# Kernel optimization log

Measured on AMD Instinct MI355X. Metric: run time of the kernel, lower is better.

The kernel has to match this reference:

```python
import jax, jax.numpy as jnp
import numpy as np


def _lstm_layer(x, W_ih, W_hh, b_ih, b_hh, reverse=False):
    """Single LSTM layer. x: [T, B, D] -> outputs [T, B, H]. PyTorch gate order i,f,g,o."""
    H = W_hh.shape[-1]
    B = x.shape[1]
    # precompute input contribution for all steps
    xg = jnp.einsum('tbd,gd->tbg', x, W_ih) + b_ih + b_hh  # [T, B, 4H]

    def step(carry, xt):
        h, c = carry
        gates = xt + h @ W_hh.T
        i, f, g, o = jnp.split(gates, 4, axis=-1)
        c = jax.nn.sigmoid(f) * c + jax.nn.sigmoid(i) * jnp.tanh(g)
        h = jax.nn.sigmoid(o) * jnp.tanh(c)
        return (h, c), h

    init = (jnp.zeros((B, H), x.dtype), jnp.zeros((B, H), x.dtype))
    _, hs = jax.lax.scan(step, init, xg, reverse=reverse)
    return hs


def setup_inputs() -> dict:
    key = jax.random.key(0)
    ks = jax.random.split(key, 24)
    B, S, L = 64, 256, 16
    VOCAB, CVOCAB, NCLS = 50000, 128, 50
    E, CE, H = 100, 50, 300
    IN0 = E + CE          # 150, bilstm layer-0 input
    IN1 = 2 * H           # 600, bilstm layer-1 input

    def u(k, shape, fan):
        lim = 1.0 / np.sqrt(fan)
        return jax.random.uniform(k, shape, jnp.float32, -lim, lim)

    inp = {
        'word_ids': jax.random.randint(ks[0], (B, S), 0, VOCAB, jnp.int32),
        'char_ids': jax.random.randint(ks[1], (B, S, L), 0, CVOCAB, jnp.int32),
        'word_embed': jax.random.normal(ks[2], (VOCAB, E), jnp.float32) * 0.1,
        'char_embed': jax.random.normal(ks[3], (CVOCAB, CE), jnp.float32) * 0.1,
        # char LSTM: 2 layers, unidirectional, input==hidden==CE -> stack over layers
        'cWih': u(ks[4], (2, 4 * CE, CE), CE),
        'cWhh': u(ks[5], (2, 4 * CE, CE), CE),
        'cbih': u(ks[6], (2, 4 * CE), CE),
        'cbhh': u(ks[7], (2, 4 * CE), CE),
        # bilstm layer 0: stack over directions [2, ...]
        'b0_Wih': u(ks[8], (2, 4 * H, IN0), H),
        'b0_Whh': u(ks[9], (2, 4 * H, H), H),
        'b0_bih': u(ks[10], (2, 4 * H), H),
        'b0_bhh': u(ks[11], (2, 4 * H), H),
        # bilstm layer 1
        'b1_Wih': u(ks[12], (2, 4 * H, IN1), H),
        'b1_Whh': u(ks[13], (2, 4 * H, H), H),
        'b1_bih': u(ks[14], (2, 4 * H), H),
        'b1_bhh': u(ks[15], (2, 4 * H), H),
        'fcW': u(ks[16], (NCLS, 2 * H), 2 * H),
        'fcb': u(ks[17], (NCLS,), 2 * H),
    }
    return inp


def reference(word_ids, char_ids, word_embed, char_embed, cWih, cWhh, cbih, cbhh,
              b0_Wih, b0_Whh, b0_bih, b0_bhh, b1_Wih, b1_Whh, b1_bih, b1_bhh,
              fcW, fcb):
    B, S, L = char_ids.shape
    CE = char_embed.shape[1]

    # --- char-level path: batch all B*S words through the 2-layer char LSTM ---
    ch = char_embed[char_ids.reshape(B * S, L)]            # [BS, L, CE]
    x = jnp.transpose(ch, (1, 0, 2))                       # [L, BS, CE]
    x = _lstm_layer(x, cWih[0], cWhh[0], cbih[0], cbhh[0])
    x = _lstm_layer(x, cWih[1], cWhh[1], cbih[1], cbhh[1])
    char_feat = x[-1].reshape(B, S, CE)                    # last step of top layer

    # --- word path + concat ---
    emb = word_embed[word_ids]                             # [B, S, E]
    seq = jnp.transpose(jnp.concatenate([emb, char_feat], axis=-1), (1, 0, 2))  # [S, B, 150]

    # --- 2-layer bidirectional LSTM ---
    f0 = _lstm_layer(seq, b0_Wih[0], b0_Whh[0], b0_bih[0], b0_bhh[0])
    r0 = _lstm_layer(seq, b0_Wih[1], b0_Whh[1], b0_bih[1], b0_bhh[1], reverse=True)
    h0 = jnp.concatenate([f0, r0], axis=-1)                # [S, B, 600]
    f1 = _lstm_layer(h0, b1_Wih[0], b1_Whh[0], b1_bih[0], b1_bhh[0])
    r1 = _lstm_layer(h0, b1_Wih[1], b1_Whh[1], b1_bih[1], b1_bhh[1], reverse=True)
    h1 = jnp.concatenate([f1, r1], axis=-1)                # [S, B, 600]

    out = jnp.einsum('sbh,ch->bsc', h1, fcW) + fcb         # [B, S, NCLS]
    return jax.nn.log_softmax(out, axis=-1)
```

## Files before the change

### kernel.cpp

```cpp
#include <hip/hip_runtime.h>

typedef unsigned short u16;
typedef unsigned int   u32;
typedef unsigned long long u64;
typedef __attribute__((ext_vector_type(8))) short bf16x8;
typedef __attribute__((ext_vector_type(4))) float f32x4;

#define MFMA16(a,b,c) __builtin_amdgcn_mfma_f32_16x16x32_bf16((a),(b),(c),0,0,0)

#define NWG   19
#define HP    320
#define GP    304
#define XGB   4096
#define SLOTS 257

static const size_t OFF_XG  = 0;
static const size_t SZ_XG   = (size_t)2*256*NWG*XGB*2;
static const size_t OFF_H0  = OFF_XG + SZ_XG;
static const size_t SZ_HB   = (size_t)2*SLOTS*64*HP*2;
static const size_t OFF_H1  = OFF_H0 + SZ_HB;
static const size_t OFF_CF  = OFF_H1 + SZ_HB;
static const size_t SZ_CF   = (size_t)16384*64*2;
static const size_t OFF_W0  = OFF_CF + SZ_CF;
static const size_t SZ_W0   = (size_t)2432*160*2;
static const size_t OFF_W1  = OFF_W0 + SZ_W0;
static const size_t SZ_W1   = (size_t)2432*640*2;
static const size_t OFF_WFC = OFF_W1 + SZ_W1;
static const size_t SZ_WFC  = (size_t)64*640*2;
static const size_t OFF_B0  = OFF_WFC + SZ_WFC;
static const size_t OFF_B1  = OFF_B0 + 2432*4;
static const size_t OFF_BFC = OFF_B1 + 2432*4;
static const size_t OFF_FL0 = OFF_BFC + 64*4;
static const size_t SZ_FL   = (size_t)2*256*NWG*4;
static const size_t OFF_FL1 = OFF_FL0 + SZ_FL;
static const size_t OFF_DT  = OFF_FL1 + SZ_FL;
static const size_t WS_NEED = OFF_DT + 4;

__device__ __forceinline__ float bf2f(u16 u){ union{u32 i; float f;} v; v.i=(u32)u<<16; return v.f; }
__device__ __forceinline__ u16 f2bf(float f){ union{float f; u32 u;} v; v.f=f; u32 r=v.u+0x7fffu+((v.u>>16)&1u); return (u16)(r>>16); }
__device__ __forceinline__ float sigf(float x){ return __builtin_amdgcn_rcpf(1.f+__builtin_amdgcn_exp2f(-1.4426950408889634f*x)); }
__device__ __forceinline__ float tanhf_(float x){ return 2.f*__builtin_amdgcn_rcpf(1.f+__builtin_amdgcn_exp2f(-2.8853900817779268f*x))-1.f; }
__device__ __forceinline__ float ldf(const void* p, size_t i, bool f32){
  return f32 ? ((const float*)p)[i] : bf2f(((const u16*)p)[i]);
}
__device__ __forceinline__ u16 ldh(const void* p, size_t i, bool f32){
  return f32 ? f2bf(((const float*)p)[i]) : ((const u16*)p)[i];
}

__global__ __launch_bounds__(256,1) void k_detect(const u16* __restrict__ probe, u32* __restrict__ cnt)
{
  int c = 0;
  for (int i = threadIdx.x; i < 65536; i += 256) {
    u16 v = probe[i];
    if (((v >> 7) & 0xFF) == 0xFF) ++c;
  }
  if (c) atomicAdd(cnt, (u32)c);
}

__global__ __launch_bounds__(256,4) void k_prep(
    const void* __restrict__ b0_Wih, const void* __restrict__ b0_bih, const void* __restrict__ b0_bhh,
    const void* __restrict__ b1_Wih, const void* __restrict__ b1_bih, const void* __restrict__ b1_bhh,
    const void* __restrict__ fcW,    const void* __restrict__ fcb,
    u16* __restrict__ W0p, u16* __restrict__ W1p, u16* __restrict__ Wfc,
    float* __restrict__ bias0, float* __restrict__ bias1, float* __restrict__ biasfc,
    const u32* __restrict__ dtf)
{
  const bool isf32 = (*dtf >= 8u);
  const int T0 = 2432*160, T1 = 2432*640, T2 = 64*640;
  const int total = T0 + T1 + T2 + 2432 + 2432 + 64;
  for (int i = blockIdx.x*256 + threadIdx.x; i < total; i += gridDim.x*256) {
    int x = i;
    if (x < T0) {
      int n = x/160, k = x%160;
      int dir = n/1216, cc = n%1216, g = cc/GP, uu = cc%GP;
      W0p[x] = (uu<300 && k<150) ? ldh(b0_Wih, ((size_t)dir*1200 + g*300 + uu)*150 + k, isf32) : (u16)0;
      continue;
    }
    x -= T0;
    if (x < T1) {
      int n = x/640, k = x%640;
      int dir = n/1216, cc = n%1216, g = cc/GP, uu = cc%GP;
      int part = (k>=320), ui = k - part*320;
      W1p[x] = (uu<300 && ui<300) ? ldh(b1_Wih, ((size_t)dir*1200 + g*300 + uu)*600 + part*300 + ui, isf32) : (u16)0;
      continue;
    }
    x -= T1;
    if (x < T2) {
      int n = x/640, k = x%640;
      int part = (k>=320), ui = k - part*320;
      Wfc[x] = (n<50 && ui<300) ? ldh(fcW, (size_t)n*600 + part*300 + ui, isf32) : (u16)0;
      continue;
    }
    x -= T2;
    if (x < 2432) {
      int dir = x/1216, cc = x%1216, g = cc/GP, uu = cc%GP;
      bias0[x] = (uu<300) ? ldf(b0_bih, dir*1200+g*300+uu, isf32) + ldf(b0_bhh, dir*1200+g*300+uu, isf32) : 0.f;
      continue;
    }
    x -= 2432;
    if (x < 2432) {
      int dir = x/1216, cc = x%1216, g = cc/GP, uu = cc%GP;
      bias1[x] = (uu<300) ? ldf(b1_bih, dir*1200+g*300+uu, isf32) + ldf(b1_bhh, dir*1200+g*300+uu, isf32) : 0.f;
      continue;
    }
    x -= 2432;
    biasfc[x] = (x<50) ? ldf(fcb, x, isf32) : 0.f;
  }
}

__global__ __launch_bounds__(256,1) void k_char(
    const int* __restrict__ char_ids, const void* __restrict__ cemb,
    const void* __restrict__ cWih, const void* __restrict__ cWhh,
    const void* __restrict__ cbih, const void* __restrict__ cbhh,
    u16* __restrict__ charfeat, const u32* __restrict__ dtf)
{
  __shared__ u16 emb[128][64];
  __shared__ int ids[16][64];
  __shared__ u16 h0s[64][64];
  __shared__ u16 h1s[64][64];
  const bool isf32 = (*dtf >= 8u);
  const int tid = threadIdx.x;
  const int g0  = blockIdx.x * 64;

  for (int e = tid; e < 128*64; e += 256) {
    int row = e>>6, col = e&63;
    (&emb[0][0])[e] = (col<50) ? ldh(cemb, row*50 + col, isf32) : (u16)0;
  }
  for (int e = tid; e < 1024; e += 256) ids[e&15][e>>4] = char_ids[(size_t)g0*16 + e];
  for (int e = tid; e < 4096; e += 256) { (&h0s[0][0])[e] = 0; (&h1s[0][0])[e] = 0; }
  __syncthreads();

  const int w = tid>>6, lane = tid&63, quad = lane>>4, lcol = lane&15;
  const int u = w*16 + lcol;

  bf16x8 Wf[2][4][4];
  #pragma unroll
  for (int l=0; l<2; ++l)
    #pragma unroll
    for (int g=0; g<4; ++g)
      #pragma unroll
      for (int kt=0; kt<4; ++kt) {
        union { bf16x8 v; u16 h[8]; } t8;
        #pragma unroll
        for (int q=0; q<8; ++q) {
          int k = kt*32 + quad*8 + q;
          u16 val = 0;
          if (u < 50) {
            if (k < 50)                  val = ldh(cWih, l*10000 + (g*50+u)*50 + k, isf32);
            else if (k >= 64 && k < 114) val = ldh(cWhh, l*10000 + (g*50+u)*50 + (k-64), isf32);
          }
          t8.h[q] = val;
        }
        Wf[l][g][kt] = t8.v;
      }
  float bs[2][4];
  #pragma unroll
  for (int l=0; l<2; ++l)
    #pragma unroll
    for (int g=0; g<4; ++g)
      bs[l][g] = (u<50) ? ldf(cbih, l*200+g*50+u, isf32) + ldf(cbhh, l*200+g*50+u, isf32) : 0.f;

  float c0[4][4] = {}; float c1[4][4] = {};
  float h0n[4][4], h1n[4][4];

  for (int t=0; t<16; ++t) {
    #pragma unroll
    for (int m=0; m<4; ++m) {
      f32x4 acc[4];
      #pragma unroll
      for (int g=0; g<4; ++g) acc[g] = (f32x4){bs[0][g], bs[0][g], bs[0][g], bs[0][g]};
      #pragma unroll
      for (int kt=0; kt<4; ++kt) {
        bf16x8 a;
        if (kt < 2) { int id = ids[t][m*16+lcol]; a = *(const bf16x8*)&emb[id][kt*32 + quad*8]; }
        else        { a = *(const bf16x8*)&h0s[m*16+lcol][(kt-2)*32 + quad*8]; }
        #pragma unroll
        for (int g=0; g<4; ++g) acc[g] = MFMA16(a, Wf[0][g][kt], acc[g]);
      }
      #pragma unroll
      for (int r=0; r<4; ++r) {
        float cn = sigf(acc[1][r])*c0[m][r] + sigf(acc[0][r])*tanhf_(acc[2][r]);
        c0[m][r] = cn;
        h0n[m][r] = sigf(acc[3][r]) * tanhf_(cn);
      }
    }
    __syncthreads();
    #pragma unroll
    for (int m=0; m<4; ++m)
      #pragma unroll
      for (int r=0; r<4; ++r) h0s[m*16 + quad*4 + r][u] = f2bf(h0n[m][r]);
    __syncthreads();
    #pragma unroll
    for (int m=0; m<4; ++m) {
      f32x4 acc[4];
      #pragma unroll
      for (int g=0; g<4; ++g) acc[g] = (f32x4){bs[1][g], bs[1][g], bs[1][g], bs[1][g]};
      #pragma unroll
      for (int kt=0; kt<4; ++kt) {
        bf16x8 a = (kt<2) ? *(const bf16x8*)&h0s[m*16+lcol][kt*32 + quad*8]
                          : *(const bf16x8*)&h1s[m*16+lcol][(kt-2)*32 + quad*8];
        #pragma unroll
        for (int g=0; g<4; ++g) acc[g] = MFMA16(a, Wf[1][g][kt], acc[g]);
      }
      #pragma unroll
      for (int r=0; r<4; ++r) {
        float cn = sigf(acc[1][r])*c1[m][r] + sigf(acc[0][r])*tanhf_(acc[2][r]);
        c1[m][r] = cn;
        h1n[m][r] = sigf(acc[3][r]) * tanhf_(cn);
      }
    }
    __syncthreads();
    #pragma unroll
    for (int m=0; m<4; ++m)
      #pragma unroll
      for (int r=0; r<4; ++r) h1s[m*16 + quad*4 + r][u] = f2bf(h1n[m][r]);
    __syncthreads();
  }
  for (int e = tid; e < 4096; e += 256)
    charfeat[(size_t)(g0 + (e>>6))*64 + (e&63)] = (&h1s[0][0])[e];
}

__device__ __forceinline__ size_t xg_addr(int n, int row){
  int dir = n/1216, cc = n%1216, g = cc/GP, cg = cc%GP, jj = cg>>4, uc = cg&15;
  int t = row>>6, b = row&63;
  return (((size_t)dir*256 + t)*NWG + jj)*XGB + (g*16 + uc)*64 + b;
}

__global__ __launch_bounds__(256,2) void k_proj0(
    const int* __restrict__ word_ids, const void* __restrict__ wemb,
    const u16* __restrict__ charfeat, const u16* __restrict__ W0p,
    const float* __restrict__ bias0, u16* __restrict__ xg, const u32* __restrict__ dtf)
{
  __shared__ u16 As[64][160];
  __shared__ u16 Bst[64][160];
  const bool isf32 = (*dtf >= 8u);
  const int tid = threadIdx.x;
  const int r0 = blockIdx.x*64, n0 = blockIdx.y*64;
  u32* Asu = (u32*)&As[0][0];
  u32* Bsu = (u32*)&Bst[0][0];
  for (int e = tid; e < 64*80; e += 256) {
    int rr = e/80, cu = e%80;
    int r = r0 + rr, t = r>>6, b = r&63;
    u32 v;
    if (cu < 50) {
      int wid = word_ids[b*256 + t];
      if (isf32) {
        const float* wf = (const float*)wemb;
        v = (u32)f2bf(wf[(size_t)wid*100 + cu*2]) | ((u32)f2bf(wf[(size_t)wid*100 + cu*2 + 1]) << 16);
      } else {
        v = ((const u32*)wemb)[(size_t)wid*50 + cu];
      }
    }
    else if (cu < 75) { v = ((const u32*)charfeat)[(size_t)r*32 + (cu-50)]; }
    else              v = 0;
    Asu[rr*80 + cu] = v;
  }
  for (int e = tid; e < 64*80; e += 256) {
    int n = e/80, cu = e%80;
    Bsu[n*80 + cu] = ((const u32*)W0p)[(size_t)(n0+n)*80 + cu];
  }
  __syncthreads();
  const int w = tid>>6, lane = tid&63, quad = lane>>4, lcol = lane&15;
  f32x4 acc[4] = {};
  #pragma unroll
  for (int kt=0; kt<5; ++kt) {
    bf16x8 a = *(const bf16x8*)&As[w*16+lcol][kt*32 + quad*8];
    #pragma unroll
    for (int nt=0; nt<4; ++nt) {
      bf16x8 bb = *(const bf16x8*)&Bst[nt*16+lcol][kt*32 + quad*8];
      acc[nt] = MFMA16(a, bb, acc[nt]);
    }
  }
  #pragma unroll
  for (int nt=0; nt<4; ++nt) {
    int n = n0 + nt*16 + lcol;
    float bia = bias0[n];
    #pragma unroll
    for (int r=0; r<4; ++r) {
      int row = r0 + w*16 + quad*4 + r;
      xg[xg_addr(n, row)] = f2bf(acc[nt][r] + bia);
    }
  }
}

__global__ __launch_bounds__(256,2) void k_proj1(
    const u16* __restrict__ Hbuf, const u16* __restrict__ W1p,
    const float* __restrict__ bias1, u16* __restrict__ xg)
{
  __shared__ u16 As[64][128];
  __shared__ u16 Bst[64][128];
  const int tid = threadIdx.x;
  const int r0 = blockIdx.x*64, n0 = blockIdx.y*64;
  const u32* Hu = (const u32*)Hbuf;
  const u32* Wu = (const u32*)W1p;
  u32* Asu = (u32*)&As[0][0];
  u32* Bsu = (u32*)&Bst[0][0];
  const int w = tid>>6, lane = tid&63, quad = lane>>4, lcol = lane&15;
  f32x4 acc[4] = {};
  for (int ch=0; ch<5; ++ch) {
    __syncthreads();
    for (int e = tid; e < 4096; e += 256) {
      int rr = e>>6, cu = e&63;
      int r = r0 + rr, t = r>>6, b = r&63;
      int kk = ch*128 + cu*2;
      int part = (kk>=320), off = kk - part*320;
      Asu[e] = Hu[(((size_t)part*SLOTS + (part ? 256-t : t+1))*64 + b)*160 + (off>>1)];
    }
    for (int e = tid; e < 4096; e += 256) {
      int n = e>>6, cu = e&63;
      Bsu[e] = Wu[(size_t)(n0+n)*320 + ch*64 + cu];
    }
    __syncthreads();
    #pragma unroll
    for (int kt=0; kt<4; ++kt) {
      bf16x8 a = *(const bf16x8*)&As[w*16+lcol][kt*32 + quad*8];
      #pragma unroll
      for (int nt=0; nt<4; ++nt) {
        bf16x8 bb = *(const bf16x8*)&Bst[nt*16+lcol][kt*32 + quad*8];
        acc[nt] = MFMA16(a, bb, acc[nt]);
      }
    }
  }
  #pragma unroll
  for (int nt=0; nt<4; ++nt) {
    int n = n0 + nt*16 + lcol;
    float bia = bias1[n];
    #pragma unroll
    for (int r=0; r<4; ++r) {
      int row = r0 + w*16 + quad*4 + r;
      xg[xg_addr(n, row)] = f2bf(acc[nt][r] + bia);
    }
  }
}

__global__ __launch_bounds__(256,1) void k_scan(
    const u16* __restrict__ xg, const void* __restrict__ Whh,
    u16* __restrict__ Hbuf, u32* __restrict__ flags, const u32* __restrict__ dtf)
{
  const bool isf32 = (*dtf >= 8u);
  const int bx = blockIdx.x;
  const int d = bx / NWG, j = bx % NWG;
  const int tid = threadIdx.x;
  const int w = tid>>6, lane = tid&63, quad = lane>>4, lcol = lane&15;
  const int u = j*16 + lcol;
  const int brow = w*16;

  bf16x8 Bf[4][10];
  #pragma unroll
  for (int g=0; g<4; ++g)
    #pragma unroll
    for (int kt=0; kt<10; ++kt) {
      union { bf16x8 v; u16 h[8]; } t8;
      #pragma unroll
      for (int q=0; q<8; ++q) {
        int k = kt*32 + quad*8 + q;
        t8.h[q] = (u < 300 && k < 300) ? ldh(Whh, ((size_t)d*1200 + g*300 + u)*300 + k, isf32) : (u16)0;
      }
      Bf[g][kt] = t8.v;
    }

  float c[4] = {0.f,0.f,0.f,0.f};
  u32* flg = flags + (size_t)d*256*NWG;

  for (int t=0; t<256; ++t) {
    const int tt = d ? (255 - t) : t;
    const volatile u64* xp = (const volatile u64*)(xg + (((size_t)d*256 + tt)*NWG + j)*XGB);
    u64 xq[4];
    #pragma unroll
    for (int g=0; g<4; ++g)
      xq[g] = xp[((g*16 + lcol)*64 + brow + quad*4) >> 2];

    if (t > 0) {
      const u32* f = flg + (t-1)*NWG;
      while (true) {
        u32 v = 4u;
        if (lane < NWG)
          v = __hip_atomic_load(f + lane, __ATOMIC_RELAXED, __HIP_MEMORY_SCOPE_AGENT);
        if (__ballot(v >= 4u) == ~0ull) break;
        __builtin_amdgcn_s_sleep(2);
      }
      asm volatile("" ::: "memory");
    }

    f32x4 acc[4];
    #pragma unroll
    for (int g=0; g<4; ++g) {
      union { u64 q; u16 h[4]; } t4; t4.q = xq[g];
      #pragma unroll
      for (int r=0; r<4; ++r) acc[g][r] = bf2f(t4.h[r]);
    }
    #pragma unroll
    for (int kt=0; kt<10; ++kt) {
      size_t base = (((size_t)d*SLOTS + t)*64 + (brow + lcol))*HP + kt*32 + quad*8;
      union { bf16x8 v; u64 q[2]; } a;
      a.q[0] = __hip_atomic_load((u64*)(Hbuf + base),     __ATOMIC_RELAXED, __HIP_MEMORY_SCOPE_AGENT);
      a.q[1] = __hip_atomic_load((u64*)(Hbuf + base + 4), __ATOMIC_RELAXED, __HIP_MEMORY_SCOPE_AGENT);
      #pragma unroll
      for (int g=0; g<4; ++g) acc[g] = MFMA16(a.v, Bf[g][kt], acc[g]);
    }
    #pragma unroll
    for (int r=0; r<4; ++r) {
      float cn = sigf(acc[1][r])*c[r] + sigf(acc[0][r])*tanhf_(acc[2][r]);
      c[r] = cn;
      float h = sigf(acc[3][r]) * tanhf_(cn);
      u32 mine = (u32)f2bf(h);
      u32 other = (u32)__shfl_xor((int)mine, 1, 64);
      if ((lcol & 1) == 0) {
        u32 word = mine | (other << 16);
        int b = brow + quad*4 + r;
        size_t e = (((size_t)d*SLOTS + (t+1))*64 + b)*HP + j*16 + lcol;
        __hip_atomic_store((u32*)(Hbuf + e), word, __ATOMIC_RELAXED, __HIP_MEMORY_SCOPE_AGENT);
      }
    }
    asm volatile("s_waitcnt vmcnt(0)" ::: "memory");
    if (lane == 0)
      __hip_atomic_fetch_add(flg + t*NWG + j, 1u, __ATOMIC_RELAXED, __HIP_MEMORY_SCOPE_AGENT);
  }
}

__global__ __launch_bounds__(256,2) void k_fc(
    const u16* __restrict__ Hbuf, const u16* __restrict__ Wfc,
    const float* __restrict__ biasfc, void* __restrict__ outv, const u32* __restrict__ dtf)
{
  __shared__ u16 As[64][128];
  __shared__ u16 Bst[64][128];
  const bool isf32 = (*dtf >= 8u);
  const int tid = threadIdx.x;
  const int r0 = blockIdx.x*64;
  const u32* Hu = (const u32*)Hbuf;
  const u32* Wu = (const u32*)Wfc;
  u32* Asu = (u32*)&As[0][0];
  u32* Bsu = (u32*)&Bst[0][0];
  const int w = tid>>6, lane = tid&63, quad = lane>>4, lcol = lane&15;
  f32x4 acc[4] = {};
  for (int ch=0; ch<5; ++ch) {
    __syncthreads();
    for (int e = tid; e < 4096; e += 256) {
      int rr = e>>6, cu = e&63;
      int r = r0 + rr, t = r>>6, b = r&63;
      int kk = ch*128 + cu*2;
      int part = (kk>=320), off = kk - part*320;
      Asu[e] = Hu[(((size_t)part*SLOTS + (part ? 256-t : t+1))*64 + b)*160 + (off>>1)];
    }
    for (int e = tid; e < 4096; e += 256) {
      int n = e>>6, cu = e&63;
      Bsu[e] = Wu[(size_t)n*320 + ch*64 + cu];
    }
    __syncthreads();
    #pragma unroll
    for (int kt=0; kt<4; ++kt) {
      bf16x8 a = *(const bf16x8*)&As[w*16+lcol][kt*32 + quad*8];
      #pragma unroll
      for (int nt=0; nt<4; ++nt) {
        bf16x8 bb = *(const bf16x8*)&Bst[nt*16+lcol][kt*32 + quad*8];
        acc[nt] = MFMA16(a, bb, acc[nt]);
      }
    }
  }
  float vals[4][4];
  #pragma unroll
  for (int nt=0; nt<4; ++nt) {
    int cc = nt*16 + lcol;
    float bia = biasfc[cc];
    #pragma unroll
    for (int r=0; r<4; ++r) vals[nt][r] = (cc < 50) ? (acc[nt][r] + bia) : -3.0e38f;
  }
  float lz[4];
  #pragma unroll
  for (int r=0; r<4; ++r) {
    float m = fmaxf(fmaxf(vals[0][r], vals[1][r]), fmaxf(vals[2][r], vals[3][r]));
    #pragma unroll
    for (int dd=1; dd<16; dd<<=1) m = fmaxf(m, __shfl_xor(m, dd, 64));
    float s = 0.f;
    #pragma unroll
    for (int nt=0; nt<4; ++nt) s += __builtin_amdgcn_exp2f((vals[nt][r]-m)*1.4426950408889634f);
    #pragma unroll
    for (int dd=1; dd<16; dd<<=1) s += __shfl_xor(s, dd, 64);
    lz[r] = m + __builtin_amdgcn_logf(s)*0.6931471805599453f;
  }
  #pragma unroll
  for (int nt=0; nt<4; ++nt) {
    int cc = nt*16 + lcol;
    if (cc < 50) {
      #pragma unroll
      for (int r=0; r<4; ++r) {
        int row = r0 + w*16 + quad*4 + r;
        int t = row>>6, b = row&63;
        size_t idx = ((size_t)b*256 + t)*50 + cc;
        float v = vals[nt][r] - lz[r];
        if (isf32) ((float*)outv)[idx] = v;
        else       ((u16*)outv)[idx] = f2bf(v);
      }
    }
  }
}

extern "C" void kernel_launch(void* const* d_in, const int* in_sizes, int n_in,
                              void* d_out, int out_size, void* d_ws, size_t ws_size,
                              hipStream_t stream) {
  (void)in_sizes; (void)n_in; (void)out_size;
  if (ws_size < WS_NEED) return;

  const int* word_ids = (const int*)d_in[0];
  const int* char_ids = (const int*)d_in[1];
  const void* wemb   = d_in[2];
  const void* cemb   = d_in[3];
  const void* cWih   = d_in[4];
  const void* cWhh   = d_in[5];
  const void* cbih   = d_in[6];
  const void* cbhh   = d_in[7];
  const void* b0_Wih = d_in[8];
  const void* b0_Whh = d_in[9];
  const void* b0_bih = d_in[10];
  const void* b0_bhh = d_in[11];
  const void* b1_Wih = d_in[12];
  const void* b1_Whh = d_in[13];
  const void* b1_bih = d_in[14];
  const void* b1_bhh = d_in[15];
  const void* fcW    = d_in[16];
  const void* fcb    = d_in[17];

  char* ws = (char*)d_ws;
  u16*   xg   = (u16*)(ws + OFF_XG);
  u16*   H0   = (u16*)(ws + OFF_H0);
  u16*   H1   = (u16*)(ws + OFF_H1);
  u16*   cf   = (u16*)(ws + OFF_CF);
  u16*   W0p  = (u16*)(ws + OFF_W0);
  u16*   W1p  = (u16*)(ws + OFF_W1);
  u16*   Wfc  = (u16*)(ws + OFF_WFC);
  float* bia0 = (float*)(ws + OFF_B0);
  float* bia1 = (float*)(ws + OFF_B1);
  float* biaf = (float*)(ws + OFF_BFC);
  u32*   fl0  = (u32*)(ws + OFF_FL0);
  u32*   fl1  = (u32*)(ws + OFF_FL1);
  u32*   dtf  = (u32*)(ws + OFF_DT);

  hipMemsetAsync(H0,                       0, (size_t)64*HP*2, stream);
  hipMemsetAsync(H0 + (size_t)SLOTS*64*HP, 0, (size_t)64*HP*2, stream);
  hipMemsetAsync(H1,                       0, (size_t)64*HP*2, stream);
  hipMemsetAsync(H1 + (size_t)SLOTS*64*HP, 0, (size_t)64*HP*2, stream);
  hipMemsetAsync(ws + OFF_FL0, 0, 2*SZ_FL + 4, stream);

  k_detect<<<1, 256, 0, stream>>>((const u16*)wemb, dtf);
  k_prep<<<7780, 256, 0, stream>>>(b0_Wih, b0_bih, b0_bhh, b1_Wih, b1_bih, b1_bhh,
                                   fcW, fcb, W0p, W1p, Wfc, bia0, bia1, biaf, dtf);
  k_char<<<256, 256, 0, stream>>>(char_ids, cemb, cWih, cWhh, cbih, cbhh, cf, dtf);
  k_proj0<<<dim3(256,38), 256, 0, stream>>>(word_ids, wemb, cf, W0p, bia0, xg, dtf);
  k_scan<<<2*NWG, 256, 0, stream>>>(xg, b0_Whh, H0, fl0, dtf);
  k_proj1<<<dim3(256,38), 256, 0, stream>>>(H0, W1p, bia1, xg);
  k_scan<<<2*NWG, 256, 0, stream>>>(xg, b1_Whh, H1, fl1, dtf);
  k_fc<<<256, 256, 0, stream>>>(H1, Wfc, biaf, d_out, dtf);
}
```

Before: 3.049 ms.

## Replace per-step flag counters with sentinel polling on hidden-state data

```diff
diff --git a/kernel.cpp b/kernel.cpp
--- a/kernel.cpp
+++ b/kernel.cpp
@@ -30,10 +30,7 @@
 static const size_t OFF_B0  = OFF_WFC + SZ_WFC;
 static const size_t OFF_B1  = OFF_B0 + 2432*4;
 static const size_t OFF_BFC = OFF_B1 + 2432*4;
-static const size_t OFF_FL0 = OFF_BFC + 64*4;
-static const size_t SZ_FL   = (size_t)2*256*NWG*4;
-static const size_t OFF_FL1 = OFF_FL0 + SZ_FL;
-static const size_t OFF_DT  = OFF_FL1 + SZ_FL;
+static const size_t OFF_DT  = OFF_BFC + 64*4;
 static const size_t WS_NEED = OFF_DT + 4;
 
 __device__ __forceinline__ float bf2f(u16 u){ union{u32 i; float f;} v; v.i=(u32)u<<16; return v.f; }
@@ -335,7 +332,7 @@
 
 __global__ __launch_bounds__(256,1) void k_scan(
     const u16* __restrict__ xg, const void* __restrict__ Whh,
-    u16* __restrict__ Hbuf, u32* __restrict__ flags, const u32* __restrict__ dtf)
+    u16* __restrict__ Hbuf, const u32* __restrict__ dtf)
 {
   const bool isf32 = (*dtf >= 8u);
   const int bx = blockIdx.x;
@@ -360,7 +357,6 @@
     }
 
   float c[4] = {0.f,0.f,0.f,0.f};
-  u32* flg = flags + (size_t)d*256*NWG;
 
   for (int t=0; t<256; ++t) {
     const int tt = d ? (255 - t) : t;
@@ -370,16 +366,22 @@
     for (int g=0; g<4; ++g)
       xq[g] = xp[((g*16 + lcol)*64 + brow + quad*4) >> 2];
 
-    if (t > 0) {
-      const u32* f = flg + (t-1)*NWG;
-      while (true) {
-        u32 v = 4u;
-        if (lane < NWG)
-          v = __hip_atomic_load(f + lane, __ATOMIC_RELAXED, __HIP_MEMORY_SCOPE_AGENT);
-        if (__ballot(v >= 4u) == ~0ull) break;
-        __builtin_amdgcn_s_sleep(2);
-      }
-      asm volatile("" ::: "memory");
+    union HU { bf16x8 v; u64 q[2]; u32 w4[4]; };
+    HU a[10];
+    const u16* hp = Hbuf + (((size_t)d*SLOTS + t)*64 + (brow + lcol))*HP + quad*8;
+    while (true) {
+      #pragma unroll
+      for (int kt=0; kt<10; ++kt) {
+        a[kt].q[0] = __hip_atomic_load((const u64*)(hp + kt*32),     __ATOMIC_RELAXED, __HIP_MEMORY_SCOPE_AGENT);
+        a[kt].q[1] = __hip_atomic_load((const u64*)(hp + kt*32 + 4), __ATOMIC_RELAXED, __HIP_MEMORY_SCOPE_AGENT);
+      }
+      u32 mx = 0u;
+      #pragma unroll
+      for (int kt=0; kt<10; ++kt)
+        #pragma unroll
+        for (int i=0; i<4; ++i) { u32 ww = a[kt].w4[i]; mx = (ww > mx) ? ww : mx; }
+      if (__ballot(mx != 0xFFFFFFFFu) == ~0ull) break;
+      __builtin_amdgcn_s_sleep(1);
     }
 
     f32x4 acc[4];
@@ -391,12 +393,8 @@
     }
     #pragma unroll
     for (int kt=0; kt<10; ++kt) {
-      size_t base = (((size_t)d*SLOTS + t)*64 + (brow + lcol))*HP + kt*32 + quad*8;
-      union { bf16x8 v; u64 q[2]; } a;
-      a.q[0] = __hip_atomic_load((u64*)(Hbuf + base),     __ATOMIC_RELAXED, __HIP_MEMORY_SCOPE_AGENT);
-      a.q[1] = __hip_atomic_load((u64*)(Hbuf + base + 4), __ATOMIC_RELAXED, __HIP_MEMORY_SCOPE_AGENT);
-      #pragma unroll
-      for (int g=0; g<4; ++g) acc[g] = MFMA16(a.v, Bf[g][kt], acc[g]);
+      #pragma unroll
+      for (int g=0; g<4; ++g) acc[g] = MFMA16(a[kt].v, Bf[g][kt], acc[g]);
     }
     #pragma unroll
     for (int r=0; r<4; ++r) {
@@ -412,9 +410,16 @@
         __hip_atomic_store((u32*)(Hbuf + e), word, __ATOMIC_RELAXED, __HIP_MEMORY_SCOPE_AGENT);
       }
     }
-    asm volatile("s_waitcnt vmcnt(0)" ::: "memory");
-    if (lane == 0)
-      __hip_atomic_fetch_add(flg + t*NWG + j, 1u, __ATOMIC_RELAXED, __HIP_MEMORY_SCOPE_AGENT);
+    if (j == NWG-1) {
+      #pragma unroll
+      for (int r=0; r<4; ++r) {
+        if ((lcol & 1) == 0) {
+          int b = brow + quad*4 + r;
+          size_t e2 = (((size_t)d*SLOTS + (t+1))*64 + b)*HP + 304 + lcol;
+          __hip_atomic_store((u32*)(Hbuf + e2), 0u, __ATOMIC_RELAXED, __HIP_MEMORY_SCOPE_AGENT);
+        }
+      }
+    }
   }
 }
 
@@ -531,23 +536,23 @@
   float* bia0 = (float*)(ws + OFF_B0);
   float* bia1 = (float*)(ws + OFF_B1);
   float* biaf = (float*)(ws + OFF_BFC);
-  u32*   fl0  = (u32*)(ws + OFF_FL0);
-  u32*   fl1  = (u32*)(ws + OFF_FL1);
   u32*   dtf  = (u32*)(ws + OFF_DT);
 
+  hipMemsetAsync(H0, 0xFF, SZ_HB, stream);
+  hipMemsetAsync(H1, 0xFF, SZ_HB, stream);
   hipMemsetAsync(H0,                       0, (size_t)64*HP*2, stream);
   hipMemsetAsync(H0 + (size_t)SLOTS*64*HP, 0, (size_t)64*HP*2, stream);
   hipMemsetAsync(H1,                       0, (size_t)64*HP*2, stream);
   hipMemsetAsync(H1 + (size_t)SLOTS*64*HP, 0, (size_t)64*HP*2, stream);
-  hipMemsetAsync(ws + OFF_FL0, 0, 2*SZ_FL + 4, stream);
+  hipMemsetAsync(dtf, 0, 4, stream);
 
   k_detect<<<1, 256, 0, stream>>>((const u16*)wemb, dtf);
   k_prep<<<7780, 256, 0, stream>>>(b0_Wih, b0_bih, b0_bhh, b1_Wih, b1_bih, b1_bhh,
                                    fcW, fcb, W0p, W1p, Wfc, bia0, bia1, biaf, dtf);
   k_char<<<256, 256, 0, stream>>>(char_ids, cemb, cWih, cWhh, cbih, cbhh, cf, dtf);
   k_proj0<<<dim3(256,38), 256, 0, stream>>>(word_ids, wemb, cf, W0p, bia0, xg, dtf);
-  k_scan<<<2*NWG, 256, 0, stream>>>(xg, b0_Whh, H0, fl0, dtf);
+  k_scan<<<2*NWG, 256, 0, stream>>>(xg, b0_Whh, H0, dtf);
   k_proj1<<<dim3(256,38), 256, 0, stream>>>(H0, W1p, bia1, xg);
-  k_scan<<<2*NWG, 256, 0, stream>>>(xg, b1_Whh, H1, fl1, dtf);
+  k_scan<<<2*NWG, 256, 0, stream>>>(xg, b1_Whh, H1, dtf);
   k_fc<<<256, 256, 0, stream>>>(H1, Wfc, biaf, d_out, dtf);
 }
```

Measured after the change: 2.910 ms. 1.05x faster.
